# Performance work log

Measured on AMD Instinct MI355X. Metric: run time of the kernel, lower is better.

## Reference

```python
import jax, jax.numpy as jnp
import numpy as np

N, H, L, K, P = 6000, 256, 10, 30, 128


def setup_inputs() -> dict:
    key = jax.random.key(0)
    ks = jax.random.split(key, 16)
    s = 0.05
    return {
        "pos": jax.random.uniform(ks[0], (N, 3), dtype=jnp.float32),
        "box": jnp.ones((3,), jnp.float32),
        "enc_W": jax.random.normal(ks[1], (3, H), jnp.float32) * s,
        "enc_b": jnp.zeros((H,), jnp.float32),
        "msg_W": jax.random.normal(ks[2], (L, 2 * H + 4, H), jnp.float32) * s,
        "msg_b": jnp.zeros((L, H), jnp.float32),
        "msg_g": jnp.ones((L, H), jnp.float32),
        "msg_beta": jnp.zeros((L, H), jnp.float32),
        "upd_W": jax.random.normal(ks[3], (L, 2 * H, H), jnp.float32) * s,
        "upd_b": jnp.zeros((L, H), jnp.float32),
        "upd_g": jnp.ones((L, H), jnp.float32),
        "upd_beta": jnp.zeros((L, H), jnp.float32),
        "proj_W1": jax.random.normal(ks[4], (H, H), jnp.float32) * s,
        "proj_b1": jnp.zeros((H,), jnp.float32),
        "proj_W2": jax.random.normal(ks[5], (H, P), jnp.float32) * s,
        "proj_b2": jnp.zeros((P,), jnp.float32),
        "k": K,
    }


def _ln(x, g, b, eps=1e-5):
    mu = jnp.mean(x, axis=-1, keepdims=True)
    var = jnp.mean((x - mu) ** 2, axis=-1, keepdims=True)
    return (x - mu) * jax.lax.rsqrt(var + eps) * g + b


def reference(pos, box, enc_W, enc_b, msg_W, msg_b, msg_g, msg_beta,
              upd_W, upd_b, upd_g, upd_beta, proj_W1, proj_b1, proj_W2, proj_b2, k):
    n = pos.shape[0]
    # PBC minimum-image displacement: disp[a, b] = pos[a] - pos[b]  -> [n, n, 3]
    disp = pos[:, None, :] - pos[None, :, :]
    disp = disp - jnp.round(disp / box) * box
    dist2 = jnp.sum(disp * disp, axis=-1)                      # [n, n]
    # exclude self (distance 0 on the diagonal), equivalent to torch topk(k+1)[:,1:]
    ar = jnp.arange(n)
    dist2 = dist2.at[ar, ar].set(1e9)
    neg, nbr = jax.lax.top_k(-dist2, k)                        # k smallest distances
    d_k = jnp.sqrt(-neg)                                       # [n, k]
    src = jnp.repeat(ar, k)                                    # [E] central particle
    dst = nbr.reshape(-1)                                      # [E] neighbor (message target)
    edge_attr = jnp.concatenate([disp[src, dst], d_k.reshape(-1, 1)], axis=1)  # [E, 4]

    counts = jax.ops.segment_sum(jnp.ones((n * k, 1), pos.dtype), dst, num_segments=n)
    denom = jnp.maximum(counts, 1.0)                           # mean aggr; 0 msgs -> 0

    h = pos @ enc_W + enc_b                                    # encoder [n, H]

    def step(h, p):
        mW, mb, mg, mbt, uW, ub, ug, ubt = p
        # PyG: x_i = x[edge_index[1]] = x[dst], x_j = x[edge_index[0]] = x[src]
        feat = jnp.concatenate([h[dst], h[src], edge_attr], axis=1)   # [E, 2H+4]
        m = _ln(jax.nn.relu(feat @ mW + mb), mg, mbt)                 # msg_mlp
        agg = jax.ops.segment_sum(m, dst, num_segments=h.shape[0]) / denom
        u = _ln(jax.nn.relu(jnp.concatenate([h, agg], axis=1) @ uW + ub), ug, ubt)
        return h + u, None

    h, _ = jax.lax.scan(step, h, (msg_W, msg_b, msg_g, msg_beta,
                                  upd_W, upd_b, upd_g, upd_beta))
    return jax.nn.relu(h @ proj_W1 + proj_b1) @ proj_W2 + proj_b2
```

## Files before the change

kernel.cpp:

```cpp
#include <hip/hip_runtime.h>

#define NN 6000
#define HH 256
#define LL 10
#define KX 30
#define PP 128
#define EE (NN * KX)
#define KPADU 512
#define RPADU 520
#define RPQ 264
#define RH 264
#define NBINS 1024
#define BINSCALE 32768.0f
#define CAP 64

typedef __attribute__((ext_vector_type(8))) short short8;
typedef __attribute__((ext_vector_type(4))) float f32x4;

__device__ __forceinline__ unsigned short f2bf(float x) {
  union { float f; unsigned u; } v; v.f = x;
  return (unsigned short)((v.u + 0x7fffu + ((v.u >> 16) & 1u)) >> 16);
}

__global__ __launch_bounds__(256) void knn_kernel(
    const float* __restrict__ pos, const float* __restrict__ box,
    int* __restrict__ nbr, float* __restrict__ ea, int* __restrict__ counts) {
  __shared__ int hist[NBINS];
  __shared__ unsigned long long cand[CAP];
  __shared__ int cnt;
  __shared__ float Tsh;
  __shared__ float wvv[4];
  __shared__ int wvi[4];
  const int a = blockIdx.x, tid = threadIdx.x;
  const int lane = tid & 63, wv = tid >> 6;
  const float bx = box[0], by = box[1], bz = box[2];
  const float pax = pos[a * 3 + 0], pay = pos[a * 3 + 1], paz = pos[a * 3 + 2];
  for (int i = tid; i < NBINS; i += 256) hist[i] = 0;
  if (tid == 0) cnt = 0;
  __syncthreads();
  float v[24];
#pragma unroll
  for (int q = 0; q < 24; ++q) {
    int j = tid + (q << 8);
    float d2 = 3e38f;
    if (j < NN && j != a) {
      float dx = pax - pos[j * 3 + 0]; dx -= rintf(dx / bx) * bx;
      float dy = pay - pos[j * 3 + 1]; dy -= rintf(dy / by) * by;
      float dz = paz - pos[j * 3 + 2]; dz -= rintf(dz / bz) * bz;
      d2 = dx * dx + dy * dy + dz * dz;
    }
    v[q] = d2;
    if (d2 < 0.03125f) atomicAdd(&hist[(int)(d2 * BINSCALE)], 1);
  }
  __syncthreads();
  if (wv == 0) {
    int loc = 0;
#pragma unroll
    for (int i = 0; i < 16; ++i) loc += hist[lane * 16 + i];
    int inc = loc;
#pragma unroll
    for (int o = 1; o < 64; o <<= 1) {
      int t = __shfl_up(inc, o, 64);
      if (lane >= o) inc += t;
    }
    unsigned long long m = __ballot(inc >= KX);
    if (m == 0) {
      if (lane == 0) Tsh = -1.f;
    } else {
      int l0 = __ffsll(m) - 1;
      if (lane == l0) {
        int run = inc - loc;
        int B = l0 * 16;
        for (int i = 0; i < 16; ++i) {
          run += hist[l0 * 16 + i];
          if (run >= KX) { B = l0 * 16 + i; break; }
        }
        Tsh = (float)(B + 1) * (1.0f / BINSCALE);
      }
    }
  }
  __syncthreads();
  const float T = Tsh;
  if (T > 0.f) {
#pragma unroll
    for (int q = 0; q < 24; ++q) {
      if (v[q] < T) {
        int idx = atomicAdd(&cnt, 1);
        if (idx < CAP)
          cand[idx] = ((unsigned long long)__float_as_uint(v[q]) << 32) |
                      (unsigned)(tid + (q << 8));
      }
    }
    __syncthreads();
  }
  const int nc = cnt;
  const bool fast = (T > 0.f) && (nc >= KX) && (nc <= CAP);
  if (fast) {
    if (wv == 0) {
      unsigned long long key = (lane < nc) ? cand[lane] : ~0ull;
#pragma unroll
      for (int k = 2; k <= 64; k <<= 1) {
#pragma unroll
        for (int j = 32; j >= 1; j >>= 1) {
          if (j >= k) continue;
          unsigned long long other = __shfl_xor(key, j, 64);
          bool lower = ((lane & j) == 0);
          bool asc = ((lane & k) == 0);
          unsigned long long mn = (key < other) ? key : other;
          unsigned long long mx = (key < other) ? other : key;
          key = (lower == asc) ? mn : mx;
        }
      }
      if (lane < KX) {
        int b = (int)(key & 0xffffffffu);
        float d2 = __uint_as_float((unsigned)(key >> 32));
        float dx = pax - pos[b * 3 + 0]; dx -= rintf(dx / bx) * bx;
        float dy = pay - pos[b * 3 + 1]; dy -= rintf(dy / by) * by;
        float dz = paz - pos[b * 3 + 2]; dz -= rintf(dz / bz) * bz;
        nbr[a * KX + lane] = b;
        float4 e4; e4.x = dx; e4.y = dy; e4.z = dz; e4.w = sqrtf(d2);
        *(float4*)&ea[(a * KX + lane) * 4] = e4;
        atomicAdd(&counts[b], 1);
      }
    }
  } else {
    float lmin = v[0]; int larg = tid;
#pragma unroll
    for (int q = 1; q < 24; ++q) {
      int j = tid + (q << 8);
      if (v[q] < lmin) { lmin = v[q]; larg = j; }
    }
    for (int r = 0; r < KX; ++r) {
      float m = lmin; int ar = larg;
#pragma unroll
      for (int o = 1; o < 64; o <<= 1) {
        float m2 = __shfl_xor(m, o, 64);
        int a2 = __shfl_xor(ar, o, 64);
        if (m2 < m || (m2 == m && a2 < ar)) { m = m2; ar = a2; }
      }
      if (lane == 0) { wvv[wv] = m; wvi[wv] = ar; }
      __syncthreads();
      float gm = wvv[0]; int ga = wvi[0];
#pragma unroll
      for (int w2 = 1; w2 < 4; ++w2) {
        float m2 = wvv[w2]; int a2 = wvi[w2];
        if (m2 < gm || (m2 == gm && a2 < ga)) { gm = m2; ga = a2; }
      }
      if (tid == 0) {
        int b = ga;
        nbr[a * KX + r] = b;
        float dx = pax - pos[b * 3 + 0]; dx -= rintf(dx / bx) * bx;
        float dy = pay - pos[b * 3 + 1]; dy -= rintf(dy / by) * by;
        float dz = paz - pos[b * 3 + 2]; dz -= rintf(dz / bz) * bz;
        float4 e4; e4.x = dx; e4.y = dy; e4.z = dz; e4.w = sqrtf(gm);
        *(float4*)&ea[(a * KX + r) * 4] = e4;
        atomicAdd(&counts[b], 1);
      }
      if ((ga & 255) == tid) {
        const int qq = ga >> 8;
#pragma unroll
        for (int q = 0; q < 24; ++q) if (q == qq) v[q] = 3e38f;
        lmin = v[0]; larg = tid;
#pragma unroll
        for (int q = 1; q < 24; ++q) {
          int j = tid + (q << 8);
          if (v[q] < lmin) { lmin = v[q]; larg = j; }
        }
      }
      __syncthreads();
    }
  }
}

__global__ __launch_bounds__(256) void offsets_kernel(
    const int* __restrict__ counts, int* __restrict__ offs, float* __restrict__ invd) {
  __shared__ int ssum[256];
  const int t = threadIdx.x;
  const int lo = t * 24;
  int hi = lo + 24; if (hi > NN) hi = NN;
  int s = 0;
  for (int i = lo; i < hi; ++i) s += counts[i];
  ssum[t] = s;
  __syncthreads();
  for (int o = 1; o < 256; o <<= 1) {
    int v2 = (t >= o) ? ssum[t - o] : 0;
    __syncthreads();
    ssum[t] += v2;
    __syncthreads();
  }
  int run = ssum[t] - s;
  for (int i = lo; i < hi; ++i) { offs[i] = run; run += counts[i]; }
  if (t == 255) offs[NN] = run;
  for (int i = t; i < NN; i += 256) {
    float c = (float)counts[i];
    invd[i] = 1.0f / fmaxf(c, 1.0f);
  }
}

__global__ __launch_bounds__(256) void scatter_kernel(
    const int* __restrict__ nbr, const int* __restrict__ offs,
    int* __restrict__ cursor, int* __restrict__ elist) {
  const int e = blockIdx.x * 256 + threadIdx.x;
  if (e >= EE) return;
  const int d = nbr[e];
  const int slot = offs[d] + atomicAdd(&cursor[d], 1);
  elist[slot] = e;
}

__global__ __launch_bounds__(256) void sortlists_kernel(
    const int* __restrict__ offs, int* __restrict__ elist) {
  const int wv = threadIdx.x >> 6, lane = threadIdx.x & 63;
  const int d = blockIdx.x * 4 + wv;
  if (d >= NN) return;
  const int s0 = offs[d], s1 = offs[d + 1];
  const int n = s1 - s0;
  if (n <= 1) return;
  if (n <= 64) {
    int key = (lane < n) ? elist[s0 + lane] : 0x7fffffff;
#pragma unroll
    for (int k = 2; k <= 64; k <<= 1) {
#pragma unroll
      for (int j = 32; j >= 1; j >>= 1) {
        if (j >= k) continue;
        int other = __shfl_xor(key, j, 64);
        bool lower = ((lane & j) == 0);
        bool asc = ((lane & k) == 0);
        int mn = (key < other) ? key : other;
        int mx = (key < other) ? other : key;
        key = (lower == asc) ? mn : mx;
      }
    }
    if (lane < n) elist[s0 + lane] = key;
  } else if (lane == 0) {
    for (int i = s0 + 1; i < s1; ++i) {
      int v = elist[i]; int j = i - 1;
      while (j >= s0 && elist[j] > v) { elist[j + 1] = elist[j]; --j; }
      elist[j + 1] = v;
    }
  }
}

__global__ __launch_bounds__(256) void wcvt_kernel(
    const float* __restrict__ W, unsigned short* __restrict__ BT,
    int K, int Kpad, int lsW, int lsBT, int rowoff) {
  __shared__ unsigned short t[64][65];
  const int l = blockIdx.x, k0 = blockIdx.y * 64, n0 = blockIdx.z * 64;
  const int tid = threadIdx.x, tc = tid & 63, tr = tid >> 6;
  const float* Wl = W + (size_t)l * lsW + (size_t)rowoff * 256;
  unsigned short* BTl = BT + (size_t)l * lsBT;
  for (int r = tr; r < 64; r += 4) {
    int k = k0 + r;
    float v = (k < K) ? Wl[(size_t)k * 256 + n0 + tc] : 0.f;
    t[r][tc] = f2bf(v);
  }
  __syncthreads();
  for (int r = tr; r < 64; r += 4) {
    int n = n0 + r, k = k0 + tc;
    if (k < Kpad) BTl[(size_t)n * Kpad + k] = t[tc][r];
  }
}

__global__ __launch_bounds__(256) void enc_kernel(
    const float* __restrict__ pos, const float* __restrict__ W,
    const float* __restrict__ b, float* __restrict__ h,
    unsigned short* __restrict__ hb) {
  const int gidx = blockIdx.x * 256 + threadIdx.x;
  const int node = gidx >> 8, c = gidx & 255;
  float v = pos[node * 3 + 0] * W[c] + pos[node * 3 + 1] * W[HH + c] +
            pos[node * 3 + 2] * W[2 * HH + c] + b[c];
  h[gidx] = v;
  hb[gidx] = f2bf(v);
}

__global__ __launch_bounds__(256, 2) void pq_mfma(
    const unsigned short* __restrict__ hb, float* __restrict__ PQ,
    const unsigned short* __restrict__ BT2, const float* __restrict__ mb) {
  __shared__ __align__(16) unsigned short A[16 * RPQ];
  const int tid = threadIdx.x;
  const int base = blockIdx.x * 16;
  const int lane = tid & 63, wv = tid >> 6;
  for (int it = 0; it < 4; ++it) {
    int row = it * 4 + wv;
    ushort4 v = *(const ushort4*)(hb + (size_t)(base + row) * HH + lane * 4);
    *(ushort4*)&A[row * RPQ + lane * 4] = v;
  }
  __syncthreads();
  const int m = lane & 15, g = lane >> 4;
  const int n0 = wv * 128;
  f32x4 acc[8] = {};
  const unsigned short* ap = A + m * RPQ + g * 8;
  const unsigned short* bp = BT2 + (size_t)(n0 + m) * 256 + g * 8;
  for (int ks = 0; ks < 8; ++ks) {
    const int ko = ks * 32;
    short8 a = *(const short8*)(ap + ko);
#pragma unroll
    for (int t = 0; t < 8; ++t)
      acc[t] = __builtin_amdgcn_mfma_f32_16x16x32_bf16(
          a, *(const short8*)(bp + (size_t)t * 16 * 256 + ko), acc[t], 0, 0, 0);
  }
#pragma unroll
  for (int t = 0; t < 8; ++t) {
    int c = n0 + t * 16 + m;
    float bias = (c < 256) ? mb[c] : 0.f;
#pragma unroll
    for (int i = 0; i < 4; ++i)
      PQ[(size_t)(base + g * 4 + i) * 512 + c] = acc[t][i] + bias;
  }
}

__global__ __launch_bounds__(256, 3) void fused_layer(
    float* __restrict__ h, unsigned short* __restrict__ hb,
    const float* __restrict__ PQin, float* __restrict__ PQout,
    const int* __restrict__ elist, const int* __restrict__ offs,
    const float* __restrict__ invd, const float* __restrict__ ea,
    const float* __restrict__ msgWl, const float* __restrict__ mg,
    const float* __restrict__ mbt,
    const unsigned short* __restrict__ uBTl, const float* __restrict__ ub,
    const float* __restrict__ ug, const float* __restrict__ ubt,
    const unsigned short* __restrict__ nextBT2,
    const float* __restrict__ nextmb, int has_next) {
  __shared__ float aggsh[8][256];
  __shared__ __align__(16) unsigned short feat[8 * RPADU];
  __shared__ __align__(16) unsigned short hsh[8 * RH];
  __shared__ float psum[8][4], psum2[8][4], smu[8], srs[8];
  const int tid = threadIdx.x;
  const int base = blockIdx.x * 8;
  {
    const int hh = tid & 31;
    const int dloc = tid >> 5;
    const int d = base + dloc;
    const int c0 = hh * 8;
    float we[4][8], gg[8], bt[8], p[8], acc8[8];
#pragma unroll
    for (int j = 0; j < 4; ++j) {
      *(float4*)&we[j][0] = *(const float4*)(msgWl + (size_t)(512 + j) * 256 + c0);
      *(float4*)&we[j][4] = *(const float4*)(msgWl + (size_t)(512 + j) * 256 + c0 + 4);
    }
    *(float4*)&gg[0] = *(const float4*)(mg + c0);
    *(float4*)&gg[4] = *(const float4*)(mg + c0 + 4);
    *(float4*)&bt[0] = *(const float4*)(mbt + c0);
    *(float4*)&bt[4] = *(const float4*)(mbt + c0 + 4);
    *(float4*)&p[0] = *(const float4*)(PQin + (size_t)d * 512 + c0);
    *(float4*)&p[4] = *(const float4*)(PQin + (size_t)d * 512 + c0 + 4);
#pragma unroll
    for (int k = 0; k < 8; ++k) acc8[k] = 0.f;
    const int s0 = offs[d], s1 = offs[d + 1];
    for (int e = s0; e < s1; ++e) {
      const int eid = elist[e];
      const int src = eid / KX;
      const float4 e4 = *(const float4*)(ea + (size_t)eid * 4);
      const float* qp = PQin + (size_t)src * 512 + 256 + c0;
      float q[8];
      *(float4*)&q[0] = *(const float4*)qp;
      *(float4*)&q[4] = *(const float4*)(qp + 4);
      float v[8], s = 0.f, s2 = 0.f;
#pragma unroll
      for (int k = 0; k < 8; ++k) {
        float z = p[k] + q[k] + e4.x * we[0][k] + e4.y * we[1][k] +
                  e4.z * we[2][k] + e4.w * we[3][k];
        z = fmaxf(z, 0.f);
        v[k] = z; s += z; s2 += z * z;
      }
#pragma unroll
      for (int o = 1; o < 32; o <<= 1) {
        s += __shfl_xor(s, o, 64);
        s2 += __shfl_xor(s2, o, 64);
      }
      const float mu = s * (1.f / HH);
      const float rs = rsqrtf(s2 * (1.f / HH) - mu * mu + 1e-5f);
#pragma unroll
      for (int k = 0; k < 8; ++k) acc8[k] += (v[k] - mu) * rs * gg[k] + bt[k];
    }
    const float iv = invd[d];
#pragma unroll
    for (int k = 0; k < 8; ++k) acc8[k] *= iv;
    *(float4*)&aggsh[dloc][c0] = *(float4*)&acc8[0];
    *(float4*)&aggsh[dloc][c0 + 4] = *(float4*)&acc8[4];
  }
  __syncthreads();
  for (int it = 0; it < 4; ++it) {
    int idx = it * 256 + tid;
    int row = idx >> 7, ps = (idx & 127) * 4;
    int node = base + row;
    ushort4 o;
    if (ps < 256) {
      o = *(const ushort4*)(hb + (size_t)node * HH + ps);
    } else {
      float4 a4 = *(const float4*)(&aggsh[row][ps - 256]);
      o.x = f2bf(a4.x); o.y = f2bf(a4.y); o.z = f2bf(a4.z); o.w = f2bf(a4.w);
    }
    *(ushort4*)&feat[row * RPADU + ps] = o;
  }
  __syncthreads();
  const int lane = tid & 63, wv = tid >> 6;
  const int m = lane & 15, g = lane >> 4;
  const int n0 = wv * 64;
  {
    f32x4 acc[4] = {};
    const unsigned short* ap = feat + (m & 7) * RPADU + g * 8;
    const unsigned short* bp0 = uBTl + (size_t)(n0 + m) * KPADU + g * 8;
    const unsigned short* bp1 = bp0 + 16 * KPADU;
    const unsigned short* bp2 = bp0 + 32 * KPADU;
    const unsigned short* bp3 = bp0 + 48 * KPADU;
    for (int ks = 0; ks < 16; ++ks) {
      const int ko = ks * 32;
      short8 a = *(const short8*)(ap + ko);
      acc[0] = __builtin_amdgcn_mfma_f32_16x16x32_bf16(a, *(const short8*)(bp0 + ko), acc[0], 0, 0, 0);
      acc[1] = __builtin_amdgcn_mfma_f32_16x16x32_bf16(a, *(const short8*)(bp1 + ko), acc[1], 0, 0, 0);
      acc[2] = __builtin_amdgcn_mfma_f32_16x16x32_bf16(a, *(const short8*)(bp2 + ko), acc[2], 0, 0, 0);
      acc[3] = __builtin_amdgcn_mfma_f32_16x16x32_bf16(a, *(const short8*)(bp3 + ko), acc[3], 0, 0, 0);
    }
    float bb[4], gg4[4], be4[4];
#pragma unroll
    for (int nt = 0; nt < 4; ++nt) {
      int c = n0 + nt * 16 + m;
      bb[nt] = ub[c]; gg4[nt] = ug[c]; be4[nt] = ubt[c];
    }
#pragma unroll
    for (int i = 0; i < 4; ++i) {
      float s = 0.f, s2 = 0.f;
#pragma unroll
      for (int nt = 0; nt < 4; ++nt) {
        float v = fmaxf(acc[nt][i] + bb[nt], 0.f);
        acc[nt][i] = v; s += v; s2 += v * v;
      }
#pragma unroll
      for (int o = 1; o < 16; o <<= 1) {
        s += __shfl_xor(s, o, 64);
        s2 += __shfl_xor(s2, o, 64);
      }
      if (m == 0 && g < 2) { int e = g * 4 + i; psum[e][wv] = s; psum2[e][wv] = s2; }
    }
    __syncthreads();
    if (tid < 8) {
      float s = psum[tid][0] + psum[tid][1] + psum[tid][2] + psum[tid][3];
      float s2 = psum2[tid][0] + psum2[tid][1] + psum2[tid][2] + psum2[tid][3];
      float mu = s * (1.f / HH);
      smu[tid] = mu;
      srs[tid] = rsqrtf(s2 * (1.f / HH) - mu * mu + 1e-5f);
    }
    __syncthreads();
    if (g < 2) {
#pragma unroll
      for (int i = 0; i < 4; ++i) {
        int e = g * 4 + i;
        int node = base + e;
        float mu = smu[e], rs = srs[e];
#pragma unroll
        for (int nt = 0; nt < 4; ++nt) {
          int c = n0 + nt * 16 + m;
          float u = (acc[nt][i] - mu) * rs * gg4[nt] + be4[nt];
          float hn = h[(size_t)node * HH + c] + u;
          h[(size_t)node * HH + c] = hn;
          unsigned short hv = f2bf(hn);
          hb[(size_t)node * HH + c] = hv;
          hsh[e * RH + c] = hv;
        }
      }
    }
  }
  if (has_next) {
    __syncthreads();
    f32x4 pacc[8] = {};
    const unsigned short* ap3 = hsh + (m & 7) * RH + g * 8;
    const unsigned short* bp3 = nextBT2 + (size_t)(wv * 128 + m) * 256 + g * 8;
    for (int ks = 0; ks < 8; ++ks) {
      const int ko = ks * 32;
      short8 a = *(const short8*)(ap3 + ko);
#pragma unroll
      for (int t = 0; t < 8; ++t)
        pacc[t] = __builtin_amdgcn_mfma_f32_16x16x32_bf16(
            a, *(const short8*)(bp3 + (size_t)t * 16 * 256 + ko), pacc[t], 0, 0, 0);
    }
    if (g < 2) {
#pragma unroll
      for (int t = 0; t < 8; ++t) {
        int c = wv * 128 + t * 16 + m;
        float bias = (c < 256) ? nextmb[c] : 0.f;
#pragma unroll
        for (int i = 0; i < 4; ++i) {
          int e = g * 4 + i;
          PQout[(size_t)(base + e) * 512 + c] = pacc[t][i] + bias;
        }
      }
    }
  }
}

#define FMA4(J, F, W) { const float _f = (F); \
  acc[J][0] += _f * (W).x; acc[J][1] += _f * (W).y; \
  acc[J][2] += _f * (W).z; acc[J][3] += _f * (W).w; }

template <int ROWLEN, int KQ>
__device__ __forceinline__ void gemm16(const float* fbase, const float* wcol,
                                       float (&acc)[4][4], const int wv) {
  const float* f0p = fbase + (size_t)wv * ROWLEN;
  const float* f1p = f0p + 4 * ROWLEN;
  const float* f2p = f0p + 8 * ROWLEN;
  const float* f3p = f0p + 12 * ROWLEN;
  const float* wr = wcol;
#pragma unroll 2
  for (int kq = 0; kq < KQ; ++kq) {
    const int kk = kq * 4;
    const float4 w0 = *(const float4*)(wr + 0 * HH);
    const float4 w1 = *(const float4*)(wr + 1 * HH);
    const float4 w2 = *(const float4*)(wr + 2 * HH);
    const float4 w3 = *(const float4*)(wr + 3 * HH);
    const float4 f0 = *(const float4*)(f0p + kk);
    const float4 f1 = *(const float4*)(f1p + kk);
    const float4 f2 = *(const float4*)(f2p + kk);
    const float4 f3 = *(const float4*)(f3p + kk);
    FMA4(0, f0.x, w0) FMA4(0, f0.y, w1) FMA4(0, f0.z, w2) FMA4(0, f0.w, w3)
    FMA4(1, f1.x, w0) FMA4(1, f1.y, w1) FMA4(1, f1.z, w2) FMA4(1, f1.w, w3)
    FMA4(2, f2.x, w0) FMA4(2, f2.y, w1) FMA4(2, f2.z, w2) FMA4(2, f2.w, w3)
    FMA4(3, f3.x, w0) FMA4(3, f3.y, w1) FMA4(3, f3.z, w2) FMA4(3, f3.w, w3)
    wr += 4 * HH;
  }
}

__global__ __launch_bounds__(256, 4) void proj_kernel(
    const float* __restrict__ h,
    const float* __restrict__ W1, const float* __restrict__ b1,
    const float* __restrict__ W2, const float* __restrict__ b2,
    float* __restrict__ out) {
  __shared__ float sh[16][256];
  __shared__ float st[16][256];
  const int tid = threadIdx.x, base = blockIdx.x * 16;
  for (int i = 0; i < 16; ++i) sh[i][tid] = h[(size_t)(base + i) * HH + tid];
  __syncthreads();
  const int lane = tid & 63, wv = tid >> 6;
  const int c4 = lane * 4;
  float acc[4][4] = {};
  gemm16<256, 64>(&sh[0][0], W1 + c4, acc, wv);
  const float4 bb = *(const float4*)(b1 + c4);
#pragma unroll
  for (int j = 0; j < 4; ++j) {
    const int e = wv + 4 * j;
    st[e][c4 + 0] = fmaxf(acc[j][0] + bb.x, 0.f);
    st[e][c4 + 1] = fmaxf(acc[j][1] + bb.y, 0.f);
    st[e][c4 + 2] = fmaxf(acc[j][2] + bb.z, 0.f);
    st[e][c4 + 3] = fmaxf(acc[j][3] + bb.w, 0.f);
  }
  __syncthreads();
  const int c2 = lane * 2;
  float a0[4] = {}, a1[4] = {};
  const float* w2p = W2 + c2;
#pragma unroll 2
  for (int kk = 0; kk < 256; ++kk) {
    const float2 w = *(const float2*)(w2p + (size_t)kk * PP);
    const float g0 = st[wv + 0][kk];
    const float g1 = st[wv + 4][kk];
    const float g2 = st[wv + 8][kk];
    const float g3 = st[wv + 12][kk];
    a0[0] += g0 * w.x; a1[0] += g0 * w.y;
    a0[1] += g1 * w.x; a1[1] += g1 * w.y;
    a0[2] += g2 * w.x; a1[2] += g2 * w.y;
    a0[3] += g3 * w.x; a1[3] += g3 * w.y;
  }
  const float2 b2v = *(const float2*)(b2 + c2);
#pragma unroll
  for (int j = 0; j < 4; ++j) {
    const int node = base + wv + 4 * j;
    out[(size_t)node * PP + c2 + 0] = a0[j] + b2v.x;
    out[(size_t)node * PP + c2 + 1] = a1[j] + b2v.y;
  }
}

extern "C" void kernel_launch(void* const* d_in, const int* in_sizes, int n_in,
                              void* d_out, int out_size, void* d_ws, size_t ws_size,
                              hipStream_t stream) {
  const float* pos   = (const float*)d_in[0];
  const float* box   = (const float*)d_in[1];
  const float* encW  = (const float*)d_in[2];
  const float* encB  = (const float*)d_in[3];
  const float* msgW  = (const float*)d_in[4];
  const float* msgB  = (const float*)d_in[5];
  const float* msgG  = (const float*)d_in[6];
  const float* msgBt = (const float*)d_in[7];
  const float* updW  = (const float*)d_in[8];
  const float* updB  = (const float*)d_in[9];
  const float* updG  = (const float*)d_in[10];
  const float* updBt = (const float*)d_in[11];
  const float* pW1   = (const float*)d_in[12];
  const float* pb1   = (const float*)d_in[13];
  const float* pW2   = (const float*)d_in[14];
  const float* pb2   = (const float*)d_in[15];
  float* out = (float*)d_out;

  char* w = (char*)d_ws;
  auto alloc = [&](size_t bytes) {
    char* p = w;
    w += (bytes + 255) & ~(size_t)255;
    return p;
  };
  int*   nbr    = (int*)alloc((size_t)EE * 4);
  float* ea     = (float*)alloc((size_t)EE * 16);
  int*   counts = (int*)alloc((size_t)NN * 4);
  int*   offs   = (int*)alloc((size_t)(NN + 1) * 4);
  int*   cursor = (int*)alloc((size_t)NN * 4);
  int*   elist  = (int*)alloc((size_t)EE * 4);
  float* invd   = (float*)alloc((size_t)NN * 4);
  float* hbuf   = (float*)alloc((size_t)NN * HH * 4);
  float* PQ0    = (float*)alloc((size_t)NN * 512 * 4);
  float* PQ1    = (float*)alloc((size_t)NN * 512 * 4);
  unsigned short* hb   = (unsigned short*)alloc((size_t)NN * HH * 2);
  unsigned short* mBT2 = (unsigned short*)alloc((size_t)LL * 512 * 256 * 2);
  unsigned short* uBT  = (unsigned short*)alloc((size_t)LL * 256 * KPADU * 2);

  hipMemsetAsync(counts, 0, (size_t)NN * 4, stream);
  hipMemsetAsync(cursor, 0, (size_t)NN * 4, stream);

  wcvt_kernel<<<dim3(LL, 4, 4), 256, 0, stream>>>(
      msgW, mBT2, 256, 256, 516 * 256, 512 * 256, 0);
  wcvt_kernel<<<dim3(LL, 4, 4), 256, 0, stream>>>(
      msgW, mBT2 + 256 * 256, 256, 256, 516 * 256, 512 * 256, 256);
  wcvt_kernel<<<dim3(LL, 8, 4), 256, 0, stream>>>(
      updW, uBT, 512, 512, 512 * 256, 256 * 512, 0);

  knn_kernel<<<NN, 256, 0, stream>>>(pos, box, nbr, ea, counts);
  offsets_kernel<<<1, 256, 0, stream>>>(counts, offs, invd);
  scatter_kernel<<<(EE + 255) / 256, 256, 0, stream>>>(nbr, offs, cursor, elist);
  sortlists_kernel<<<(NN + 3) / 4, 256, 0, stream>>>(offs, elist);
  enc_kernel<<<NN, 256, 0, stream>>>(pos, encW, encB, hbuf, hb);
  pq_mfma<<<NN / 16, 256, 0, stream>>>(hb, PQ0, mBT2, msgB);

  for (int l = 0; l < LL; ++l) {
    const int hn = (l + 1 < LL) ? 1 : 0;
    float* PQin  = (l & 1) ? PQ1 : PQ0;
    float* PQout = (l & 1) ? PQ0 : PQ1;
    fused_layer<<<NN / 8, 256, 0, stream>>>(
        hbuf, hb, PQin, PQout, elist, offs, invd, ea,
        msgW + (size_t)l * 516 * 256,
        msgG + (size_t)l * HH, msgBt + (size_t)l * HH,
        uBT + (size_t)l * 256 * KPADU,
        updB + (size_t)l * HH, updG + (size_t)l * HH, updBt + (size_t)l * HH,
        mBT2 + (size_t)(hn ? (l + 1) : 0) * 512 * 256,
        msgB + (size_t)(hn ? (l + 1) : 0) * HH, hn);
  }
  proj_kernel<<<NN / 16, 256, 0, stream>>>(hbuf, pW1, pb1, pW2, pb2, out);
}
```

Baseline: 1.095 ms.

## Split fused layer into edge-parallel message kernel and separate MFMA update kernel

The per-layer fused kernel is split in two. The message aggregation now runs in its own kernel, where each destination node's incoming edges are spread across 4 thread groups, with two-deep software prefetch of edge attributes and source rows and a reduction of the partial sums through shared memory. The update/next-PQ MFMA kernel then reads the aggregate from a new global buffer. The aim is more parallelism and latency hiding on the irregular gather, paid for with an extra global round trip for the aggregate and an extra launch per layer.

Result: no change. 1.087 ms (-0.7%).

```diff
diff --git a/kernel.cpp b/kernel.cpp
--- a/kernel.cpp
+++ b/kernel.cpp
@@ -13,6 +13,8 @@
 #define NBINS 1024
 #define BINSCALE 32768.0f
 #define CAP 64
+#define ESPL 4
+#define DPB 2
 
 typedef __attribute__((ext_vector_type(8))) short short8;
 typedef __attribute__((ext_vector_type(4))) float f32x4;
@@ -308,76 +310,107 @@
   }
 }
 
-__global__ __launch_bounds__(256, 3) void fused_layer(
-    float* __restrict__ h, unsigned short* __restrict__ hb,
-    const float* __restrict__ PQin, float* __restrict__ PQout,
+__global__ __launch_bounds__(256) void msg_edge(
+    const float* __restrict__ PQin, float* __restrict__ agg,
     const int* __restrict__ elist, const int* __restrict__ offs,
     const float* __restrict__ invd, const float* __restrict__ ea,
     const float* __restrict__ msgWl, const float* __restrict__ mg,
-    const float* __restrict__ mbt,
+    const float* __restrict__ mbt) {
+  __shared__ float part[DPB][ESPL][256];
+  const int tid = threadIdx.x;
+  const int hh = tid & 31;
+  const int gid = tid >> 5;
+  const int dl = gid >> 2;
+  const int sp = gid & 3;
+  const int d = blockIdx.x * DPB + dl;
+  const int c0 = hh * 8;
+  float we[4][8], gg[8], bt[8], p[8], acc8[8];
+#pragma unroll
+  for (int j = 0; j < 4; ++j) {
+    *(float4*)&we[j][0] = *(const float4*)(msgWl + (size_t)(512 + j) * 256 + c0);
+    *(float4*)&we[j][4] = *(const float4*)(msgWl + (size_t)(512 + j) * 256 + c0 + 4);
+  }
+  *(float4*)&gg[0] = *(const float4*)(mg + c0);
+  *(float4*)&gg[4] = *(const float4*)(mg + c0 + 4);
+  *(float4*)&bt[0] = *(const float4*)(mbt + c0);
+  *(float4*)&bt[4] = *(const float4*)(mbt + c0 + 4);
+  *(float4*)&p[0] = *(const float4*)(PQin + (size_t)d * 512 + c0);
+  *(float4*)&p[4] = *(const float4*)(PQin + (size_t)d * 512 + c0 + 4);
+#pragma unroll
+  for (int k = 0; k < 8; ++k) acc8[k] = 0.f;
+  const int s0 = offs[d];
+  const int n = offs[d + 1] - s0;
+  float4 eaA = {0, 0, 0, 0}, qA0 = {0, 0, 0, 0}, qA1 = {0, 0, 0, 0};
+  float4 eaB = {0, 0, 0, 0}, qB0 = {0, 0, 0, 0}, qB1 = {0, 0, 0, 0};
+  if (sp < n) {
+    int eid = elist[s0 + sp];
+    eaA = *(const float4*)(ea + (size_t)eid * 4);
+    const float* qp = PQin + (size_t)(eid / KX) * 512 + 256 + c0;
+    qA0 = *(const float4*)qp; qA1 = *(const float4*)(qp + 4);
+  }
+  if (sp + ESPL < n) {
+    int eid = elist[s0 + sp + ESPL];
+    eaB = *(const float4*)(ea + (size_t)eid * 4);
+    const float* qp = PQin + (size_t)(eid / KX) * 512 + 256 + c0;
+    qB0 = *(const float4*)qp; qB1 = *(const float4*)(qp + 4);
+  }
+  for (int e = sp; e < n; e += ESPL) {
+    float4 eaC = {0, 0, 0, 0}, qC0 = {0, 0, 0, 0}, qC1 = {0, 0, 0, 0};
+    int eC = e + 2 * ESPL;
+    if (eC < n) {
+      int eid = elist[s0 + eC];
+      eaC = *(const float4*)(ea + (size_t)eid * 4);
+      const float* qp = PQin + (size_t)(eid / KX) * 512 + 256 + c0;
+      qC0 = *(const float4*)qp; qC1 = *(const float4*)(qp + 4);
+    }
+    float q[8];
+    *(float4*)&q[0] = qA0; *(float4*)&q[4] = qA1;
+    float v[8], s = 0.f, s2 = 0.f;
+#pragma unroll
+    for (int k = 0; k < 8; ++k) {
+      float z = p[k] + q[k] + eaA.x * we[0][k] + eaA.y * we[1][k] +
+                eaA.z * we[2][k] + eaA.w * we[3][k];
+      z = fmaxf(z, 0.f);
+      v[k] = z; s += z; s2 += z * z;
+    }
+#pragma unroll
+    for (int o = 1; o < 32; o <<= 1) {
+      s += __shfl_xor(s, o, 64);
+      s2 += __shfl_xor(s2, o, 64);
+    }
+    const float mu = s * (1.f / HH);
+    const float rs = rsqrtf(s2 * (1.f / HH) - mu * mu + 1e-5f);
+#pragma unroll
+    for (int k = 0; k < 8; ++k) acc8[k] += (v[k] - mu) * rs * gg[k] + bt[k];
+    eaA = eaB; qA0 = qB0; qA1 = qB1;
+    eaB = eaC; qB0 = qC0; qB1 = qC1;
+  }
+  *(float4*)&part[dl][sp][c0] = *(float4*)&acc8[0];
+  *(float4*)&part[dl][sp][c0 + 4] = *(float4*)&acc8[4];
+  __syncthreads();
+  if (sp == 0) {
+    const float iv = invd[d];
+#pragma unroll
+    for (int k = 0; k < 8; ++k) {
+      int c = c0 + k;
+      float sval = ((part[dl][0][c] + part[dl][1][c]) + part[dl][2][c]) + part[dl][3][c];
+      agg[(size_t)d * 256 + c] = sval * iv;
+    }
+  }
+}
+
+__global__ __launch_bounds__(256, 3) void updpq_mfma(
+    float* __restrict__ h, unsigned short* __restrict__ hb,
+    const float* __restrict__ agg, float* __restrict__ PQout,
     const unsigned short* __restrict__ uBTl, const float* __restrict__ ub,
     const float* __restrict__ ug, const float* __restrict__ ubt,
     const unsigned short* __restrict__ nextBT2,
     const float* __restrict__ nextmb, int has_next) {
-  __shared__ float aggsh[8][256];
   __shared__ __align__(16) unsigned short feat[8 * RPADU];
   __shared__ __align__(16) unsigned short hsh[8 * RH];
   __shared__ float psum[8][4], psum2[8][4], smu[8], srs[8];
   const int tid = threadIdx.x;
   const int base = blockIdx.x * 8;
-  {
-    const int hh = tid & 31;
-    const int dloc = tid >> 5;
-    const int d = base + dloc;
-    const int c0 = hh * 8;
-    float we[4][8], gg[8], bt[8], p[8], acc8[8];
-#pragma unroll
-    for (int j = 0; j < 4; ++j) {
-      *(float4*)&we[j][0] = *(const float4*)(msgWl + (size_t)(512 + j) * 256 + c0);
-      *(float4*)&we[j][4] = *(const float4*)(msgWl + (size_t)(512 + j) * 256 + c0 + 4);
-    }
-    *(float4*)&gg[0] = *(const float4*)(mg + c0);
-    *(float4*)&gg[4] = *(const float4*)(mg + c0 + 4);
-    *(float4*)&bt[0] = *(const float4*)(mbt + c0);
-    *(float4*)&bt[4] = *(const float4*)(mbt + c0 + 4);
-    *(float4*)&p[0] = *(const float4*)(PQin + (size_t)d * 512 + c0);
-    *(float4*)&p[4] = *(const float4*)(PQin + (size_t)d * 512 + c0 + 4);
-#pragma unroll
-    for (int k = 0; k < 8; ++k) acc8[k] = 0.f;
-    const int s0 = offs[d], s1 = offs[d + 1];
-    for (int e = s0; e < s1; ++e) {
-      const int eid = elist[e];
-      const int src = eid / KX;
-      const float4 e4 = *(const float4*)(ea + (size_t)eid * 4);
-      const float* qp = PQin + (size_t)src * 512 + 256 + c0;
-      float q[8];
-      *(float4*)&q[0] = *(const float4*)qp;
-      *(float4*)&q[4] = *(const float4*)(qp + 4);
-      float v[8], s = 0.f, s2 = 0.f;
-#pragma unroll
-      for (int k = 0; k < 8; ++k) {
-        float z = p[k] + q[k] + e4.x * we[0][k] + e4.y * we[1][k] +
-                  e4.z * we[2][k] + e4.w * we[3][k];
-        z = fmaxf(z, 0.f);
-        v[k] = z; s += z; s2 += z * z;
-      }
-#pragma unroll
-      for (int o = 1; o < 32; o <<= 1) {
-        s += __shfl_xor(s, o, 64);
-        s2 += __shfl_xor(s2, o, 64);
-      }
-      const float mu = s * (1.f / HH);
-      const float rs = rsqrtf(s2 * (1.f / HH) - mu * mu + 1e-5f);
-#pragma unroll
-      for (int k = 0; k < 8; ++k) acc8[k] += (v[k] - mu) * rs * gg[k] + bt[k];
-    }
-    const float iv = invd[d];
-#pragma unroll
-    for (int k = 0; k < 8; ++k) acc8[k] *= iv;
-    *(float4*)&aggsh[dloc][c0] = *(float4*)&acc8[0];
-    *(float4*)&aggsh[dloc][c0 + 4] = *(float4*)&acc8[4];
-  }
-  __syncthreads();
   for (int it = 0; it < 4; ++it) {
     int idx = it * 256 + tid;
     int row = idx >> 7, ps = (idx & 127) * 4;
@@ -386,7 +419,7 @@
     if (ps < 256) {
       o = *(const ushort4*)(hb + (size_t)node * HH + ps);
     } else {
-      float4 a4 = *(const float4*)(&aggsh[row][ps - 256]);
+      float4 a4 = *(const float4*)(agg + (size_t)node * HH + (ps - 256));
       o.x = f2bf(a4.x); o.y = f2bf(a4.y); o.z = f2bf(a4.z); o.w = f2bf(a4.w);
     }
     *(ushort4*)&feat[row * RPADU + ps] = o;
@@ -601,6 +634,7 @@
   int*   elist  = (int*)alloc((size_t)EE * 4);
   float* invd   = (float*)alloc((size_t)NN * 4);
   float* hbuf   = (float*)alloc((size_t)NN * HH * 4);
+  float* agg    = (float*)alloc((size_t)NN * HH * 4);
   float* PQ0    = (float*)alloc((size_t)NN * 512 * 4);
   float* PQ1    = (float*)alloc((size_t)NN * 512 * 4);
   unsigned short* hb   = (unsigned short*)alloc((size_t)NN * HH * 2);
@@ -628,10 +662,12 @@
     const int hn = (l + 1 < LL) ? 1 : 0;
     float* PQin  = (l & 1) ? PQ1 : PQ0;
     float* PQout = (l & 1) ? PQ0 : PQ1;
-    fused_layer<<<NN / 8, 256, 0, stream>>>(
-        hbuf, hb, PQin, PQout, elist, offs, invd, ea,
+    msg_edge<<<NN / DPB, 256, 0, stream>>>(
+        PQin, agg, elist, offs, invd, ea,
         msgW + (size_t)l * 516 * 256,
-        msgG + (size_t)l * HH, msgBt + (size_t)l * HH,
+        msgG + (size_t)l * HH, msgBt + (size_t)l * HH);
+    updpq_mfma<<<NN / 8, 256, 0, stream>>>(
+        hbuf, hb, agg, PQout,
         uBT + (size_t)l * 256 * KPADU,
         updB + (size_t)l * HH, updG + (size_t)l * HH, updBt + (size_t)l * HH,
         mBT2 + (size_t)(hn ? (l + 1) : 0) * 512 * 256,
```
